# Optimization experiments

Measured on AMD Instinct MI355X. Metric: run time of the kernel, lower is better.

The kernel has to match this reference:

```python
import jax, jax.numpy as jnp
import numpy as np

INIT_MEAN = 0.3


def _loo_sum(x, idx, n_seg):
    # leave-one-out segment sum along edge axis; x: [B, E]
    tot = jnp.zeros((x.shape[0], n_seg), x.dtype).at[:, idx].add(x)
    return tot[:, idx] - x


def _check_node_process(x, chk_idx, n_checks):
    # 2*atanh( prod_{e' in check, e'!=e} tanh(x_e'/2) ) via log-magnitude + sign
    t = jnp.tanh(0.5 * x)
    abs_t = jnp.clip(jnp.abs(t), 1e-12, None)
    log_loo = _loo_sum(jnp.log(abs_t), chk_idx, n_checks)
    neg = (t < 0).astype(x.dtype)
    neg_loo = _loo_sum(neg, chk_idx, n_checks)
    sign = 1.0 - 2.0 * jnp.mod(neg_loo, 2.0)
    prod = jnp.clip(sign * jnp.exp(log_loo), -1.0 + 1e-7, 1.0 - 1e-7)
    return 2.0 * jnp.arctanh(prod)


def setup_inputs() -> dict:
    N, M, DV, DC, ITERS, B = 8192, 4096, 3, 6, 5, 1024
    E = N * DV
    rng = np.random.RandomState(0)
    # regular (3,6) Tanner graph: each variable has 3 edges, each check 6
    var_idx = np.repeat(np.arange(N, dtype=np.int32), DV)
    chk_idx = rng.permutation(np.repeat(np.arange(M, dtype=np.int32), DC)).astype(np.int32)
    key = jax.random.key(0)
    k1, k2, k3 = jax.random.split(key, 3)
    llr = jax.random.normal(k1, (B, N), dtype=jnp.float32)
    vnode_w = INIT_MEAN + 0.02 * jax.random.normal(k2, (ITERS, E), dtype=jnp.float32)
    cnode_w = INIT_MEAN + 0.02 * jax.random.normal(k3, (ITERS, E), dtype=jnp.float32)
    return {
        "llr": llr,
        "vnode_w": vnode_w,
        "cnode_w": cnode_w,
        "var_idx": jnp.asarray(var_idx),
        "chk_idx": jnp.asarray(chk_idx),
        "n_checks": M,
    }


def reference(llr, vnode_w, cnode_w, var_idx, chk_idx, n_checks):
    B, N = llr.shape
    iters = vnode_w.shape[0]
    scattered_llr = llr[:, var_idx]            # [B, E]
    ext = jnp.zeros_like(scattered_llr)
    outs = []
    for i in range(iters):
        a_priori = _loo_sum(ext, var_idx, N) * vnode_w[i]
        ext = _check_node_process(a_priori + scattered_llr, chk_idx, n_checks) * cnode_w[i]
        out = jnp.zeros((B, N), llr.dtype).at[:, var_idx].add(ext) + llr
        outs.append(out)
    return jnp.stack(outs)  # [iters, B, N]
```

## Files before the change

### kernel.cpp

```cpp
#include <hip/hip_runtime.h>


#define N_VARS 8192
#define M_CHK  4096
#define ITERS  5
#define BATCH  1024
#define NEDGE  (N_VARS * 3)
#define TPB    1024
#define EPT    (NEDGE / TPB)
#define VPT    (N_VARS / TPB)
#define CPT    (M_CHK / TPB)
#define CSTRIDE 7
#define NGRP   (16 * 24)

#define LOG2E_F 1.44269504f
#define LN2_F   0.69314718f
#define E_CLIP  0.99999988f

__device__ __forceinline__ float tanh_half(float x) {
    float a  = fabsf(x);
    float ee = __builtin_amdgcn_exp2f(-a * LOG2E_F);
    float tt = (1.0f - ee) * __builtin_amdgcn_rcpf(1.0f + ee);
    unsigned sg = __float_as_uint(x) & 0x80000000u;
    return __uint_as_float(__float_as_uint(tt) | sg);
}

__device__ __forceinline__ float atanh2(float p) {
    p = fminf(fmaxf(p, -E_CLIP), E_CLIP);
    return LN2_F * (__builtin_amdgcn_logf(1.0f + p)
                  - __builtin_amdgcn_logf(1.0f - p));
}

__global__ void build_ce(const int* __restrict__ chk,
                         int* __restrict__ ce,
                         int* __restrict__ cnt) {
    int e = blockIdx.x * 256 + threadIdx.x;
    if (e < NEDGE) {
        int c = chk[e];
        int r = atomicAdd(&cnt[c], 1);
        ce[c * 6 + r] = e;
    }
}

__global__ __launch_bounds__(1024)
void assign_slots(const int* __restrict__ ce,
                  unsigned* __restrict__ tbl) {
    __shared__ unsigned gcnt[NGRP * 32];
    const int tid = threadIdx.x;
    for (int i = tid; i < NGRP * 32; i += 1024)
        gcnt[i] = 0;
    __syncthreads();
#pragma unroll
    for (int k = 0; k < M_CHK / 1024; ++k) {
        const int c = tid + k * 1024;
        const int cbase = c * CSTRIDE;
        unsigned avail = 0x3Fu;
        for (int r = 0; r < 6; ++r) {
            int e = ce[c * 6 + r];
            int t = e / 24;
            int g = (t >> 6) * 24 + (e - t * 24);
            int best = -1;
            unsigned bestc = ~0u;
#pragma unroll
            for (int s = 0; s < 6; ++s) {
                if ((avail >> s) & 1u) {
                    unsigned cc = gcnt[g * 32 + ((cbase + s) & 31)];
                    if (cc < bestc) { bestc = cc; best = s; }
                }
            }
            atomicAdd(&gcnt[g * 32 + ((cbase + best) & 31)], 1u);
            avail &= ~(1u << best);
            tbl[e] = (unsigned)(cbase + best);
        }
    }
}

__global__ void __launch_bounds__(TPB, 4)
nsp_kernel(const float* __restrict__ llr,
           const float* __restrict__ vw,
           const float* __restrict__ cw,
           const unsigned* __restrict__ tbl,
           float* __restrict__ out)
{
    __shared__ float lds_m[M_CHK * CSTRIDE];

    const int b  = blockIdx.x;
    const int t  = threadIdx.x;
    const int e0 = t * EPT;
    const int n0 = t * VPT;

    float llr_v[VPT];
    {
        const float4* p = (const float4*)(llr + (size_t)b * N_VARS + n0);
        float4 a = p[0], c = p[1];
        llr_v[0] = a.x; llr_v[1] = a.y; llr_v[2] = a.z; llr_v[3] = a.w;
        llr_v[4] = c.x; llr_v[5] = c.y; llr_v[6] = c.z; llr_v[7] = c.w;
    }

    unsigned pa[EPT / 2];
    {
        const uint4* p = (const uint4*)(tbl + e0);
#pragma unroll
        for (int k = 0; k < EPT / 4; ++k) {
            uint4 v = p[k];
            pa[2 * k]     = v.x | (v.y << 16);
            pa[2 * k + 1] = v.z | (v.w << 16);
        }
    }
#define ADDR(e) ((pa[(e) >> 1] >> (((e) & 1) * 16)) & 0xFFFFu)

    auto computeA4 = [&](int v0, const float* cwr, const float* vwr,
                         float* op, const float* rr) {
        float outb[4];
#pragma unroll
        for (int vv = 0; vv < 4; ++vv) {
            const int v = v0 + vv;
            float x0 = rr[3 * v + 0] * cwr[3 * v + 0];
            float x1 = rr[3 * v + 1] * cwr[3 * v + 1];
            float x2 = rr[3 * v + 2] * cwr[3 * v + 2];
            float s  = x0 + x1 + x2;
            outb[vv] = s + llr_v[v];
#pragma unroll
            for (int j = 0; j < 3; ++j) {
                const int e = 3 * v + j;
                float extj = (j == 0) ? x0 : (j == 1) ? x1 : x2;
                float x = (s - extj) * vwr[e] + llr_v[v];
                lds_m[ADDR(e)] = tanh_half(x);
            }
        }
        *((float4*)(op + v0)) = make_float4(outb[0], outb[1], outb[2], outb[3]);
    };

    for (int it = 0; it < ITERS; ++it) {
        if (it == 0) {
#pragma unroll
            for (int v = 0; v < VPT; ++v) {
                float p = tanh_half(llr_v[v]);
#pragma unroll
                for (int j = 0; j < 3; ++j)
                    lds_m[ADDR(3 * v + j)] = p;
            }
        } else {
            const float* cwr = cw + (size_t)(it - 1) * NEDGE + e0;
            const float* vwr = vw + (size_t)it * NEDGE + e0;
            float* op = out + ((size_t)(it - 1) * BATCH + b) * N_VARS + n0;
            float rr[EPT];
#pragma unroll
            for (int e = 0; e < EPT; ++e)
                rr[e] = lds_m[ADDR(e)];
            computeA4(0, cwr, vwr, op, rr);
            computeA4(4, cwr, vwr, op, rr);
        }
        __syncthreads();

        {
            float tv[CPT][6];
#pragma unroll
            for (int k = 0; k < CPT; ++k) {
                const int base = (t + k * TPB) * CSTRIDE;
#pragma unroll
                for (int i = 0; i < 6; ++i)
                    tv[k][i] = lds_m[base + i];
            }
#pragma unroll
            for (int k = 0; k < CPT; ++k) {
                const int base = (t + k * TPB) * CSTRIDE;
                float t0 = tv[k][0], t1 = tv[k][1], t2 = tv[k][2];
                float t3 = tv[k][3], t4 = tv[k][4], t5 = tv[k][5];
                float p1 = t0 * t1;
                float p2 = p1 * t2;
                float p3 = p2 * t3;
                float p4 = p3 * t4;
                float s4 = t5 * t4;
                float s3 = s4 * t3;
                float s2 = s3 * t2;
                float s1 = s2 * t1;
                lds_m[base + 0] = atanh2(s1);
                lds_m[base + 1] = atanh2(t0 * s2);
                lds_m[base + 2] = atanh2(p1 * s3);
                lds_m[base + 3] = atanh2(p2 * s4);
                lds_m[base + 4] = atanh2(p3 * t5);
                lds_m[base + 5] = atanh2(p4);
            }
        }
        __syncthreads();
    }

    {
        const float* cwr = cw + (size_t)(ITERS - 1) * NEDGE + e0;
        float* op = out + ((size_t)(ITERS - 1) * BATCH + b) * N_VARS + n0;
        float rr[EPT];
#pragma unroll
        for (int e = 0; e < EPT; ++e)
            rr[e] = lds_m[ADDR(e)];
        float outb[VPT];
#pragma unroll
        for (int v = 0; v < VPT; ++v) {
            outb[v] = rr[3 * v + 0] * cwr[3 * v + 0]
                    + rr[3 * v + 1] * cwr[3 * v + 1]
                    + rr[3 * v + 2] * cwr[3 * v + 2]
                    + llr_v[v];
        }
        ((float4*)op)[0] = make_float4(outb[0], outb[1], outb[2], outb[3]);
        ((float4*)op)[1] = make_float4(outb[4], outb[5], outb[6], outb[7]);
    }
#undef ADDR
}

extern "C" void kernel_launch(void* const* d_in, const int* in_sizes, int n_in,
                              void* d_out, int out_size, void* d_ws, size_t ws_size,
                              hipStream_t stream) {
    const float* llr = (const float*)d_in[0];
    const float* vw  = (const float*)d_in[1];
    const float* cw  = (const float*)d_in[2];
    const int*   chk = (const int*)d_in[4];
    float* out = (float*)d_out;

    unsigned* tbl = (unsigned*)d_ws;
    int*      cnt = (int*)((char*)d_ws + NEDGE * sizeof(unsigned));
    int*      ce  = (int*)((char*)d_ws + NEDGE * sizeof(unsigned)
                                       + M_CHK * sizeof(int));

    hipMemsetAsync(cnt, 0, M_CHK * sizeof(int), stream);
    build_ce<<<(NEDGE + 255) / 256, 256, 0, stream>>>(chk, ce, cnt);
    assign_slots<<<1, 1024, 0, stream>>>(ce, tbl);
    nsp_kernel<<<BATCH, TPB, 0, stream>>>(llr, vw, cw, tbl, out);
}
```

Measured before the change: 325.0 us.

## Store check-node messages in LDS as 16-bit fixed point and fp16

Tanh messages are quantized to int16 fixed point and check-node outputs to fp16. Each check's six messages are packed into one 16-byte LDS slot, and the slot assignment is remapped for the new stride. This shrinks the shared buffer from ~112KB to 64KB so more blocks can reside per CU, and the launch bounds are raised to match. It loses precision, which may hurt agreement with the float reference, and the tighter register budget may cause spills.

```diff
diff --git a/kernel.cpp b/kernel.cpp
--- a/kernel.cpp
+++ b/kernel.cpp
@@ -1,4 +1,5 @@
 #include <hip/hip_runtime.h>
+#include <hip/hip_fp16.h>
 
 
 #define N_VARS 8192
@@ -10,12 +11,13 @@
 #define EPT    (NEDGE / TPB)
 #define VPT    (N_VARS / TPB)
 #define CPT    (M_CHK / TPB)
-#define CSTRIDE 7
-#define NGRP   (16 * 24)
-
-#define LOG2E_F 1.44269504f
-#define LN2_F   0.69314718f
-#define E_CLIP  0.99999988f
+
+#define LOG2E_F  1.44269504f
+#define LN2_F    0.69314718f
+#define E_CLIP   0.99999988f
+#define T_SCALE  32768.0f
+#define T_CLAMP  32767.0f
+#define P_UNSCALE 2.6469779601696886e-23f
 
 __device__ __forceinline__ float tanh_half(float x) {
     float a  = fabsf(x);
@@ -23,6 +25,11 @@
     float tt = (1.0f - ee) * __builtin_amdgcn_rcpf(1.0f + ee);
     unsigned sg = __float_as_uint(x) & 0x80000000u;
     return __uint_as_float(__float_as_uint(tt) | sg);
+}
+
+__device__ __forceinline__ short quant_t(float t) {
+    float tq = fminf(fmaxf(t * T_SCALE, -T_CLAMP), T_CLAMP);
+    return (short)(int)__builtin_rintf(tq);
 }
 
 __device__ __forceinline__ float atanh2(float p) {
@@ -42,6 +49,7 @@
     }
 }
 
+#define NGRP (16 * 24)
 __global__ __launch_bounds__(1024)
 void assign_slots(const int* __restrict__ ce,
                   unsigned* __restrict__ tbl) {
@@ -50,10 +58,11 @@
     for (int i = tid; i < NGRP * 32; i += 1024)
         gcnt[i] = 0;
     __syncthreads();
+    const int POS[6] = {0, 1, 2, 4, 5, 6};
 #pragma unroll
     for (int k = 0; k < M_CHK / 1024; ++k) {
         const int c = tid + k * 1024;
-        const int cbase = c * CSTRIDE;
+        const int cbase = c * 8;
         unsigned avail = 0x3Fu;
         for (int r = 0; r < 6; ++r) {
             int e = ce[c * 6 + r];
@@ -64,25 +73,29 @@
 #pragma unroll
             for (int s = 0; s < 6; ++s) {
                 if ((avail >> s) & 1u) {
-                    unsigned cc = gcnt[g * 32 + ((cbase + s) & 31)];
+                    unsigned bk = ((unsigned)(cbase + POS[s]) >> 1) & 31u;
+                    unsigned cc = gcnt[g * 32 + bk];
                     if (cc < bestc) { bestc = cc; best = s; }
                 }
             }
-            atomicAdd(&gcnt[g * 32 + ((cbase + best) & 31)], 1u);
+            unsigned bk = ((unsigned)(cbase + POS[best]) >> 1) & 31u;
+            atomicAdd(&gcnt[g * 32 + bk], 1u);
             avail &= ~(1u << best);
-            tbl[e] = (unsigned)(cbase + best);
-        }
-    }
-}
-
-__global__ void __launch_bounds__(TPB, 4)
+            tbl[e] = (unsigned)(cbase + POS[best]);
+        }
+    }
+}
+
+__global__ void __launch_bounds__(TPB, 8)
 nsp_kernel(const float* __restrict__ llr,
            const float* __restrict__ vw,
            const float* __restrict__ cw,
            const unsigned* __restrict__ tbl,
            float* __restrict__ out)
 {
-    __shared__ float lds_m[M_CHK * CSTRIDE];
+    __shared__ uint4 lds_q[M_CHK];
+    short*        ls16 = (short*)lds_q;
+    const __half* lhf  = (const __half*)lds_q;
 
     const int b  = blockIdx.x;
     const int t  = threadIdx.x;
@@ -125,7 +138,7 @@
                 const int e = 3 * v + j;
                 float extj = (j == 0) ? x0 : (j == 1) ? x1 : x2;
                 float x = (s - extj) * vwr[e] + llr_v[v];
-                lds_m[ADDR(e)] = tanh_half(x);
+                ls16[ADDR(e)] = quant_t(tanh_half(x));
             }
         }
         *((float4*)(op + v0)) = make_float4(outb[0], outb[1], outb[2], outb[3]);
@@ -135,10 +148,10 @@
         if (it == 0) {
 #pragma unroll
             for (int v = 0; v < VPT; ++v) {
-                float p = tanh_half(llr_v[v]);
+                short q = quant_t(tanh_half(llr_v[v]));
 #pragma unroll
                 for (int j = 0; j < 3; ++j)
-                    lds_m[ADDR(3 * v + j)] = p;
+                    ls16[ADDR(3 * v + j)] = q;
             }
         } else {
             const float* cwr = cw + (size_t)(it - 1) * NEDGE + e0;
@@ -147,26 +160,26 @@
             float rr[EPT];
 #pragma unroll
             for (int e = 0; e < EPT; ++e)
-                rr[e] = lds_m[ADDR(e)];
+                rr[e] = __half2float(lhf[ADDR(e)]);
             computeA4(0, cwr, vwr, op, rr);
             computeA4(4, cwr, vwr, op, rr);
         }
         __syncthreads();
 
         {
-            float tv[CPT][6];
+            uint4 dv[CPT];
+#pragma unroll
+            for (int k = 0; k < CPT; ++k)
+                dv[k] = lds_q[t + k * TPB];
 #pragma unroll
             for (int k = 0; k < CPT; ++k) {
-                const int base = (t + k * TPB) * CSTRIDE;
-#pragma unroll
-                for (int i = 0; i < 6; ++i)
-                    tv[k][i] = lds_m[base + i];
-            }
-#pragma unroll
-            for (int k = 0; k < CPT; ++k) {
-                const int base = (t + k * TPB) * CSTRIDE;
-                float t0 = tv[k][0], t1 = tv[k][1], t2 = tv[k][2];
-                float t3 = tv[k][3], t4 = tv[k][4], t5 = tv[k][5];
+                const uint4 d = dv[k];
+                float t0 = (float)((short)(d.x));
+                float t1 = (float)((short)(d.x >> 16));
+                float t2 = (float)((short)(d.y));
+                float t3 = (float)((short)(d.z));
+                float t4 = (float)((short)(d.z >> 16));
+                float t5 = (float)((short)(d.w));
                 float p1 = t0 * t1;
                 float p2 = p1 * t2;
                 float p3 = p2 * t3;
@@ -175,12 +188,20 @@
                 float s3 = s4 * t3;
                 float s2 = s3 * t2;
                 float s1 = s2 * t1;
-                lds_m[base + 0] = atanh2(s1);
-                lds_m[base + 1] = atanh2(t0 * s2);
-                lds_m[base + 2] = atanh2(p1 * s3);
-                lds_m[base + 3] = atanh2(p2 * s4);
-                lds_m[base + 4] = atanh2(p3 * t5);
-                lds_m[base + 5] = atanh2(p4);
+                float r0 = atanh2(s1 * P_UNSCALE);
+                float r1 = atanh2(t0 * s2 * P_UNSCALE);
+                float r2 = atanh2(p1 * s3 * P_UNSCALE);
+                float r3 = atanh2(p2 * s4 * P_UNSCALE);
+                float r4 = atanh2(p3 * t5 * P_UNSCALE);
+                float r5 = atanh2(p4 * P_UNSCALE);
+                uint4 w;
+                w.x = (unsigned)__half_as_ushort(__float2half_rn(r0))
+                    | ((unsigned)__half_as_ushort(__float2half_rn(r1)) << 16);
+                w.y = (unsigned)__half_as_ushort(__float2half_rn(r2));
+                w.z = (unsigned)__half_as_ushort(__float2half_rn(r3))
+                    | ((unsigned)__half_as_ushort(__float2half_rn(r4)) << 16);
+                w.w = (unsigned)__half_as_ushort(__float2half_rn(r5));
+                lds_q[t + k * TPB] = w;
             }
         }
         __syncthreads();
@@ -192,7 +213,7 @@
         float rr[EPT];
 #pragma unroll
         for (int e = 0; e < EPT; ++e)
-            rr[e] = lds_m[ADDR(e)];
+            rr[e] = __half2float(lhf[ADDR(e)]);
         float outb[VPT];
 #pragma unroll
         for (int v = 0; v < VPT; ++v) {
```

New measurement: 537.9 us. 1.65x slower.
